# Optimization experiments

Measured on AMD Instinct MI355X. Metric: run time of the kernel, lower is better.

The kernel has to match this reference:

```python
import jax, jax.numpy as jnp
import numpy as np
import math

B, S, D, H, HD, W, G = 2, 4096, 768, 12, 64, 256, 64  # batch, seq, embed, heads, head_dim, one-sided window, n global tokens


def _chunk_keys(k, w):
    # k: [B,S,H,HD] -> overlapping 3w-wide key windows per w-sized query chunk: [B,nc,3w,H,HD]
    Bz, S_, Hh, HDd = k.shape
    nc = S_ // w
    kp = jnp.pad(k, ((0, 0), (w, w), (0, 0), (0, 0)))
    kb = kp.reshape(Bz, nc + 2, w, Hh, HDd)
    return jnp.concatenate([kb[:, 0:nc], kb[:, 1:nc + 1], kb[:, 2:nc + 2]], axis=2)


def _band_qk(q, k, w):
    # banded scores: out[b,i,h,j] = q_i . k_{i+j-w}, j in [0, 2w]
    Bz, S_, Hh, HDd = q.shape
    nc = S_ // w
    qc = q.reshape(Bz, nc, w, Hh, HDd)
    kc = _chunk_keys(k, w)
    sc = jnp.einsum('bcphd,bckhd->bchpk', qc, kc)  # [B,nc,H,w,3w]
    rows = jnp.arange(w)[:, None]
    cols = rows + jnp.arange(2 * w + 1)[None, :]   # within-window key index = p + j
    band = sc[:, :, :, rows, cols]                 # [B,nc,H,w,2w+1]
    return band.transpose(0, 1, 3, 2, 4).reshape(Bz, S_, Hh, 2 * w + 1)


def _band_pv(p, v, w):
    # out[b,i,h,:] = sum_j p[b,i,h,j] * v[b, i+j-w, h, :]
    Bz, S_, Hh, K = p.shape
    HDd = v.shape[-1]
    nc = S_ // w
    pc = p.reshape(Bz, nc, w, Hh, K).transpose(0, 1, 3, 2, 4)  # [B,nc,H,w,2w+1]
    rows = jnp.arange(w)[:, None]
    cols = rows + jnp.arange(2 * w + 1)[None, :]
    full = jnp.zeros((Bz, nc, Hh, w, 3 * w), p.dtype).at[:, :, :, rows, cols].set(pc)
    vc = _chunk_keys(v, w)
    out = jnp.einsum('bchpk,bckhd->bcphd', full, vc)  # [B,nc,w,H,HD]
    return out.reshape(Bz, S_, Hh, HDd)


def setup_inputs() -> dict:
    key = jax.random.key(0)
    ks = jax.random.split(key, 4)
    std = 0.02
    # attention mask: +1 = global (first G tokens), 0 = local windowed, no padding
    attention_mask = jnp.concatenate(
        [jnp.ones((B, G), jnp.int32), jnp.zeros((B, S - G), jnp.int32)], axis=1)
    return {
        'hidden_states': jax.random.normal(ks[0], (B, S, D), jnp.float32),
        'attention_mask': attention_mask,
        'Wq': jax.random.normal(ks[1], (D, D), jnp.float32) * std,
        'bq': jnp.zeros((D,), jnp.float32),
        'Wk': jax.random.normal(ks[2], (D, D), jnp.float32) * std,
        'bk': jnp.zeros((D,), jnp.float32),
        'Wv': jax.random.normal(ks[3], (D, D), jnp.float32) * std,
        'bv': jnp.zeros((D,), jnp.float32),
    }


def reference(hidden_states, attention_mask, Wq, bq, Wk, bk, Wv, bv):
    Bz, S_, D_ = hidden_states.shape
    HDd = D_ // H
    q = ((hidden_states @ Wq.T + bq) / math.sqrt(HDd)).reshape(Bz, S_, H, HDd)
    k = (hidden_states @ Wk.T + bk).reshape(Bz, S_, H, HDd)
    v = (hidden_states @ Wv.T + bv).reshape(Bz, S_, H, HDd)

    band = _band_qk(q, k, W)  # [B,S,H,2W+1]

    i = jnp.arange(S_)
    key_abs = i[:, None] + jnp.arange(2 * W + 1)[None, :] - W  # [S,2W+1]
    valid = (key_abs >= 0) & (key_abs < S_)
    kac = jnp.clip(key_abs, 0, S_ - 1)
    is_glob = attention_mask != 0                       # [B,S]
    glob_at_key = is_glob[:, kac] & valid[None]          # [B,S,2W+1]
    # remove global keys from windowed attention: d_mask = -10000 * head_dim (ones @ float_mask)
    band = band + jnp.where(glob_at_key, jnp.float32(-10000.0 * HDd), jnp.float32(0.0))[:, :, None, :]
    # mask_invalid_locations: out-of-range diagonals -> -inf
    band = jnp.where(valid[None, :, None, :], band, -jnp.inf)

    # global-token attention (first G tokens are the global ones)
    gs = jnp.einsum('bihd,bghd->bihg', q, k[:, :G])      # [B,S,H,G]

    scores = jnp.concatenate([gs, band], axis=-1)        # [B,S,H,G+2W+1]
    probs = jax.nn.softmax(scores.astype(jnp.float32), axis=-1)

    attn = jnp.einsum('bihg,bghd->bihd', probs[..., :G], v[:, :G]) + _band_pv(probs[..., G:], v, W)
    # [B,S,H,HD] -> (seq_len, bsz, embed_dim) as in the torch module
    return jnp.transpose(attn, (1, 0, 2, 3)).reshape(S_, Bz, D_)
```

## Files before the change

kernel.cpp:

```cpp
#include <hip/hip_runtime.h>
#include <hip/hip_bf16.h>
#include <stdint.h>

typedef __attribute__((ext_vector_type(4))) float          f32x4;
typedef __attribute__((ext_vector_type(4))) float          f4;
typedef __attribute__((ext_vector_type(2))) unsigned int   u32x2;
typedef __bf16 bf16_t;
typedef __attribute__((ext_vector_type(8))) bf16_t         bf16x8;
typedef __attribute__((ext_vector_type(8))) unsigned short u16x8;
typedef __attribute__((ext_vector_type(4))) unsigned short u16x4;

#define NB 2
#define NS 4096
#define ND 768
#define NH 12
#define NW 256

__device__ __forceinline__ unsigned short f2bf(float f) {
  union { float f; unsigned u; } v; v.f = f;
  unsigned r = v.u + 0x7fffu + ((v.u >> 16) & 1u);
  return (unsigned short)(r >> 16);
}

__device__ __forceinline__ void gload16(const void* g, void* l) {
  __builtin_amdgcn_global_load_lds((const __attribute__((address_space(1))) void*)g,
                                   (__attribute__((address_space(3))) void*)l, 16, 0, 0);
}

__global__ void cast_kernel(const float* __restrict__ in, unsigned short* __restrict__ out, int n4) {
  int i = blockIdx.x * blockDim.x + threadIdx.x;
  int stride = gridDim.x * blockDim.x;
  for (; i < n4; i += stride) {
    f4 v = reinterpret_cast<const f4*>(in)[i];
    unsigned u0 = (unsigned)f2bf(v.x) | ((unsigned)f2bf(v.y) << 16);
    unsigned u1 = (unsigned)f2bf(v.z) | ((unsigned)f2bf(v.w) << 16);
    u32x2 o = {u0, u1};
    reinterpret_cast<u32x2*>(out)[i] = o;
  }
}

__global__ void cast3_kernel(const float* __restrict__ w0, const float* __restrict__ w1,
                             const float* __restrict__ w2, unsigned short* __restrict__ o0,
                             unsigned short* __restrict__ o1, unsigned short* __restrict__ o2) {
  const int n4 = 768 * 768 / 4;
  int i = blockIdx.x * blockDim.x + threadIdx.x;
  int stride = gridDim.x * blockDim.x;
  for (; i < 3 * n4; i += stride) {
    int m = i / n4, j = i - m * n4;
    const float* in = (m == 0) ? w0 : ((m == 1) ? w1 : w2);
    unsigned short* out = (m == 0) ? o0 : ((m == 1) ? o1 : o2);
    f4 v = reinterpret_cast<const f4*>(in)[j];
    unsigned u0 = (unsigned)f2bf(v.x) | ((unsigned)f2bf(v.y) << 16);
    unsigned u1 = (unsigned)f2bf(v.z) | ((unsigned)f2bf(v.w) << 16);
    u32x2 o = {u0, u1};
    reinterpret_cast<u32x2*>(out)[j] = o;
  }
}

__global__ __launch_bounds__(256) void qkv_gemm(
    const unsigned short* __restrict__ Ab,
    const unsigned short* __restrict__ Wqb,
    const unsigned short* __restrict__ Wkb,
    const unsigned short* __restrict__ Wvb,
    const float* __restrict__ bqp, const float* __restrict__ bkp, const float* __restrict__ bvp,
    unsigned short* __restrict__ Qw, unsigned short* __restrict__ Kw, unsigned short* __restrict__ Vw) {
  __shared__ unsigned short As[128 * 32];
  __shared__ unsigned short Bs[128 * 32];

  int phys = blockIdx.x;
  int logical = (phys & 7) * 144 + (phys >> 3);
  int bn = logical % 18, bm = logical / 18;
  int mat = bn / 6, bnn = bn % 6;
  const unsigned short* Wm = (mat == 0) ? Wqb : ((mat == 1) ? Wkb : Wvb);
  const float* bias = (mat == 0) ? bqp : ((mat == 1) ? bkp : bvp);
  unsigned short* dst = (mat == 0) ? Qw : ((mat == 1) ? Kw : Vw);

  int t = threadIdx.x;
  int w = t >> 6, l = t & 63;
  int lg = l >> 4, ln = l & 15;
  int wm = w & 1, wn = w >> 1;

  f32x4 acc[4][4];
#pragma unroll
  for (int i = 0; i < 4; i++)
#pragma unroll
    for (int j = 0; j < 4; j++) acc[i][j] = f32x4{0.f, 0.f, 0.f, 0.f};

  for (int kt = 0; kt < 24; ++kt) {
    __syncthreads();
#pragma unroll
    for (int is = 0; is < 2; ++is) {
      int chunk = is * 256 + t;
      int row = chunk >> 2;
      int c8 = (chunk & 3) * 8;
      gload16(Ab + ((size_t)(bm * 128 + row)) * 768 + kt * 32 + c8, As + chunk * 8);
      gload16(Wm + ((size_t)(bnn * 128 + row)) * 768 + kt * 32 + c8, Bs + chunk * 8);
    }
    __syncthreads();
    bf16x8 af[4], bfr[4];
#pragma unroll
    for (int i = 0; i < 4; i++) {
      af[i]  = *reinterpret_cast<const bf16x8*>(As + (wm * 64 + i * 16 + ln) * 32 + lg * 8);
      bfr[i] = *reinterpret_cast<const bf16x8*>(Bs + (wn * 64 + i * 16 + ln) * 32 + lg * 8);
    }
#pragma unroll
    for (int i = 0; i < 4; i++)
#pragma unroll
      for (int j = 0; j < 4; j++)
        acc[i][j] = __builtin_amdgcn_mfma_f32_16x16x32_bf16(af[i], bfr[j], acc[i][j], 0, 0, 0);
  }

#pragma unroll
  for (int j = 0; j < 4; j++) {
    int col = bnn * 128 + wn * 64 + j * 16 + ln;
    float bv_ = bias[col];
    int hh = col >> 6, dd = col & 63;
#pragma unroll
    for (int i = 0; i < 4; i++) {
#pragma unroll
      for (int r = 0; r < 4; r++) {
        int tok = bm * 128 + wm * 64 + i * 16 + lg * 4 + r;
        int bb = tok >> 12, ss = tok & 4095;
        float v = acc[i][j][r] + bv_;
        if (mat == 0) v *= 0.125f;
        dst[(((size_t)bb * 12 + hh) * 4096 + ss) * 64 + dd] = f2bf(v);
      }
    }
  }
}

__global__ __launch_bounds__(512) void attn_kernel(
    const unsigned short* __restrict__ Qw,
    const unsigned short* __restrict__ Kw,
    const unsigned short* __restrict__ Vw,
    const int* __restrict__ amask,
    float* __restrict__ out) {
  __shared__ unsigned short Ks[2][64 * 64];
  __shared__ unsigned short Vt[2][64 * 64];
  __shared__ unsigned short Ps[8][16 * 72];
  __shared__ unsigned Msk[128];

  int phys = blockIdx.x;
  int logical = (phys & 7) * 96 + (phys >> 3);
  int qc = logical & 31;
  int bh = logical >> 5;
  int b = bh / 12;
  int hh = bh % 12;
  int qbase = qc * 128;

  int t = threadIdx.x, w = t >> 6, l = t & 63;
  int lg = l >> 4, ln = l & 15;

  const unsigned short* Qbh = Qw + (size_t)bh * (NS * 64);
  const unsigned short* Kbh = Kw + (size_t)bh * (NS * 64);
  const unsigned short* Vbh = Vw + (size_t)bh * (NS * 64);
  const int* mrow = amask + b * NS;

#pragma unroll
  for (int r8 = 0; r8 < 8; ++r8) {
    int wp = r8 * 8 + w;
    unsigned long long bal = __ballot(mrow[wp * 64 + l] != 0);
    if (l == 0) {
      Msk[wp * 2] = (unsigned)bal;
      Msk[wp * 2 + 1] = (unsigned)(bal >> 32);
    }
  }

  bf16x8 qf[2];
  {
    const unsigned short* qp = Qbh + (size_t)(qbase + w * 16 + ln) * 64 + lg * 8;
    qf[0] = *reinterpret_cast<const bf16x8*>(qp);
    qf[1] = *reinterpret_cast<const bf16x8*>(qp + 32);
  }

  float m_r[4] = {-1e30f, -1e30f, -1e30f, -1e30f};
  float l_r[4] = {0.f, 0.f, 0.f, 0.f};
  f32x4 oacc[4];
#pragma unroll
  for (int i = 0; i < 4; i++) oacc[i] = f32x4{0.f, 0.f, 0.f, 0.f};

  int q0 = qbase + w * 16 + lg * 4;

  int tt_lo = (qbase >= 256) ? 0 : ((256 - qbase) >> 6);
  int tt_hi_raw = (NS + 192 - qbase) >> 6;
  int tt_hi = tt_hi_raw < 9 ? tt_hi_raw : 9;
  int ntl = tt_hi - tt_lo + 2;

  int krow = t >> 3, gran = t & 7;
  int p2 = t & 31, d0v = (t >> 5) * 4;

  {
    gload16(Kbh + (size_t)krow * 64 + (gran ^ (krow & 7)) * 8, &Ks[0][0] + t * 8);
    const unsigned short* vp0 = Vbh + (size_t)(2 * p2) * 64 + d0v;
    u16x4 va = *reinterpret_cast<const u16x4*>(vp0);
    u16x4 vb = *reinterpret_cast<const u16x4*>(vp0 + 64);
#pragma unroll
    for (int j = 0; j < 4; ++j) {
      int d = d0v + j;
      unsigned val = (unsigned)va[j] | ((unsigned)vb[j] << 16);
      *reinterpret_cast<unsigned*>(&Vt[0][0] + d * 64 + ((2 * p2) ^ ((d & 7) << 3))) = val;
    }
  }
  __syncthreads();

  for (int idx = 0; idx < ntl; ++idx) {
    int cur = idx & 1;
    int key0 = (idx == 0) ? 0 : (qbase - 256 + (tt_lo + idx - 1) * 64);
    bool has_next = (idx + 1) < ntl;

    u16x4 va, vb;
    if (has_next) {
      int nk0 = qbase - 256 + (tt_lo + idx) * 64;
      gload16(Kbh + (size_t)(nk0 + krow) * 64 + (gran ^ (krow & 7)) * 8,
              &Ks[cur ^ 1][0] + t * 8);
      const unsigned short* vp0 = Vbh + (size_t)(nk0 + 2 * p2) * 64 + d0v;
      va = *reinterpret_cast<const u16x4*>(vp0);
      vb = *reinterpret_cast<const u16x4*>(vp0 + 64);
    }

    const unsigned short* ksb = &Ks[cur][0];
    f32x4 sa[4];
#pragma unroll
    for (int nt = 0; nt < 4; nt++) sa[nt] = f32x4{0.f, 0.f, 0.f, 0.f};
#pragma unroll
    for (int nt = 0; nt < 4; nt++) {
      int key = nt * 16 + ln;
#pragma unroll
      for (int ks = 0; ks < 2; ++ks) {
        int dby = (ks * 64 + lg * 16) ^ ((key & 7) << 4);
        bf16x8 kf = *reinterpret_cast<const bf16x8*>(ksb + key * 64 + (dby >> 1));
        sa[nt] = __builtin_amdgcn_mfma_f32_16x16x32_bf16(qf[ks], kf, sa[nt], 0, 0, 0);
      }
    }

    if (idx > 0) {
#pragma unroll
      for (int nt = 0; nt < 4; nt++) {
        int ka = key0 + nt * 16 + ln;
        bool sup = (Msk[ka >> 5] >> (ka & 31)) & 1;
#pragma unroll
        for (int r = 0; r < 4; r++) {
          bool bad = sup || ((unsigned)(ka - (q0 + r) + NW) > 2u * NW);
          if (bad) sa[nt][r] = -1e30f;
        }
      }
    }

    float scl[4];
#pragma unroll
    for (int r = 0; r < 4; r++) {
      float v = fmaxf(fmaxf(sa[0][r], sa[1][r]), fmaxf(sa[2][r], sa[3][r]));
      v = fmaxf(v, __shfl_xor(v, 1, 64));
      v = fmaxf(v, __shfl_xor(v, 2, 64));
      v = fmaxf(v, __shfl_xor(v, 4, 64));
      v = fmaxf(v, __shfl_xor(v, 8, 64));
      float mn = fmaxf(m_r[r], v);
      scl[r] = __expf(m_r[r] - mn);
      m_r[r] = mn;
    }
#pragma unroll
    for (int r = 0; r < 4; r++) {
      float s = 0.f;
#pragma unroll
      for (int nt = 0; nt < 4; nt++) {
        float p = __expf(sa[nt][r] - m_r[r]);
        sa[nt][r] = p;
        s += p;
      }
      s += __shfl_xor(s, 1, 64);
      s += __shfl_xor(s, 2, 64);
      s += __shfl_xor(s, 4, 64);
      s += __shfl_xor(s, 8, 64);
      l_r[r] = l_r[r] * scl[r] + s;
    }
#pragma unroll
    for (int nt = 0; nt < 4; nt++)
#pragma unroll
      for (int r = 0; r < 4; r++) oacc[nt][r] *= scl[r];

    unsigned short* pw = &Ps[w][0];
#pragma unroll
    for (int nt = 0; nt < 4; nt++)
#pragma unroll
      for (int r = 0; r < 4; r++) {
        __hip_bfloat16 hb = __float2bfloat16(sa[nt][r]);
        pw[(lg * 4 + r) * 72 + nt * 16 + ln] = *reinterpret_cast<unsigned short*>(&hb);
      }

    const unsigned short* vtb = &Vt[cur][0];
#pragma unroll
    for (int ks = 0; ks < 2; ++ks) {
      bf16x8 pf = *reinterpret_cast<const bf16x8*>(pw + ln * 72 + ks * 32 + lg * 8);
#pragma unroll
      for (int nt = 0; nt < 4; ++nt) {
        int d = nt * 16 + ln;
        int eoff = (ks * 32 + lg * 8) ^ ((d & 7) << 3);
        bf16x8 vf = *reinterpret_cast<const bf16x8*>(vtb + d * 64 + eoff);
        oacc[nt] = __builtin_amdgcn_mfma_f32_16x16x32_bf16(pf, vf, oacc[nt], 0, 0, 0);
      }
    }

    if (has_next) {
      unsigned short* vtn = &Vt[cur ^ 1][0];
#pragma unroll
      for (int j = 0; j < 4; ++j) {
        int d = d0v + j;
        unsigned val = (unsigned)va[j] | ((unsigned)vb[j] << 16);
        *reinterpret_cast<unsigned*>(vtn + d * 64 + ((2 * p2) ^ ((d & 7) << 3))) = val;
      }
    }
    __syncthreads();
  }

#pragma unroll
  for (int nt = 0; nt < 4; nt++) {
    int d = nt * 16 + ln;
#pragma unroll
    for (int r = 0; r < 4; r++) {
      int qa = q0 + r;
      out[((size_t)qa * NB + b) * ND + hh * 64 + d] = oacc[nt][r] / l_r[r];
    }
  }
}

extern "C" void kernel_launch(void* const* d_in, const int* in_sizes, int n_in,
                              void* d_out, int out_size, void* d_ws, size_t ws_size,
                              hipStream_t stream) {
  (void)in_sizes; (void)n_in; (void)out_size; (void)ws_size;
  const float* hidden = (const float*)d_in[0];
  const int*   amask  = (const int*)d_in[1];
  const float* Wq = (const float*)d_in[2];
  const float* bq = (const float*)d_in[3];
  const float* Wk = (const float*)d_in[4];
  const float* bk = (const float*)d_in[5];
  const float* Wv = (const float*)d_in[6];
  const float* bv = (const float*)d_in[7];
  float* out = (float*)d_out;

  char* p = (char*)d_ws;
  unsigned short* hb  = (unsigned short*)p; p += (size_t)8192 * 768 * 2;
  unsigned short* wqb = (unsigned short*)p; p += (size_t)768 * 768 * 2;
  unsigned short* wkb = (unsigned short*)p; p += (size_t)768 * 768 * 2;
  unsigned short* wvb = (unsigned short*)p; p += (size_t)768 * 768 * 2;
  unsigned short* Qws = (unsigned short*)p; p += (size_t)24 * 4096 * 64 * 2;
  unsigned short* Kws = (unsigned short*)p; p += (size_t)24 * 4096 * 64 * 2;
  unsigned short* Vws = (unsigned short*)p; p += (size_t)24 * 4096 * 64 * 2;

  cast_kernel<<<1024, 256, 0, stream>>>(hidden, hb, 8192 * 768 / 4);
  cast3_kernel<<<432, 256, 0, stream>>>(Wq, Wk, Wv, wqb, wkb, wvb);
  qkv_gemm<<<64 * 18, 256, 0, stream>>>(hb, wqb, wkb, wvb, bq, bk, bv, Qws, Kws, Vws);
  attn_kernel<<<24 * 32, 512, 0, stream>>>(Qws, Kws, Vws, amask, out);
}
```

Before: 209.7 us.

## Transpose attention MFMAs to keep P in registers and skip clean masks

Swaps MFMA operands so each lane owns one query row. Softmax stats become per-lane scalars, and P can be packed to bf16 in registers and fed to the PV MFMA without the LDS round trip. It folds log2(e) into the Q scale to use exp2f, adds a lazy rescale that only updates the running max when it grows by more than 8, and skips per-element masking for key tiles fully inside the window with no global keys. Output is written as float4 rows. The lazy-rescale threshold and the bf16 P values are numerics risks, and V reads become two 8-byte LDS loads instead of one 16-byte load.

```diff
diff --git a/kernel.cpp b/kernel.cpp
--- a/kernel.cpp
+++ b/kernel.cpp
@@ -22,6 +22,10 @@
   return (unsigned short)(r >> 16);
 }
 
+__device__ __forceinline__ unsigned pack2bf(float a, float b) {
+  return (unsigned)f2bf(a) | ((unsigned)f2bf(b) << 16);
+}
+
 __device__ __forceinline__ void gload16(const void* g, void* l) {
   __builtin_amdgcn_global_load_lds((const __attribute__((address_space(1))) void*)g,
                                    (__attribute__((address_space(3))) void*)l, 16, 0, 0);
@@ -32,9 +36,7 @@
   int stride = gridDim.x * blockDim.x;
   for (; i < n4; i += stride) {
     f4 v = reinterpret_cast<const f4*>(in)[i];
-    unsigned u0 = (unsigned)f2bf(v.x) | ((unsigned)f2bf(v.y) << 16);
-    unsigned u1 = (unsigned)f2bf(v.z) | ((unsigned)f2bf(v.w) << 16);
-    u32x2 o = {u0, u1};
+    u32x2 o = {pack2bf(v.x, v.y), pack2bf(v.z, v.w)};
     reinterpret_cast<u32x2*>(out)[i] = o;
   }
 }
@@ -50,9 +52,7 @@
     const float* in = (m == 0) ? w0 : ((m == 1) ? w1 : w2);
     unsigned short* out = (m == 0) ? o0 : ((m == 1) ? o1 : o2);
     f4 v = reinterpret_cast<const f4*>(in)[j];
-    unsigned u0 = (unsigned)f2bf(v.x) | ((unsigned)f2bf(v.y) << 16);
-    unsigned u1 = (unsigned)f2bf(v.z) | ((unsigned)f2bf(v.w) << 16);
-    u32x2 o = {u0, u1};
+    u32x2 o = {pack2bf(v.x, v.y), pack2bf(v.z, v.w)};
     reinterpret_cast<u32x2*>(out)[j] = o;
   }
 }
@@ -122,7 +122,7 @@
         int tok = bm * 128 + wm * 64 + i * 16 + lg * 4 + r;
         int bb = tok >> 12, ss = tok & 4095;
         float v = acc[i][j][r] + bv_;
-        if (mat == 0) v *= 0.125f;
+        if (mat == 0) v *= 0.1803368801111244f;
         dst[(((size_t)bb * 12 + hh) * 4096 + ss) * 64 + dd] = f2bf(v);
       }
     }
@@ -137,7 +137,6 @@
     float* __restrict__ out) {
   __shared__ unsigned short Ks[2][64 * 64];
   __shared__ unsigned short Vt[2][64 * 64];
-  __shared__ unsigned short Ps[8][16 * 72];
   __shared__ unsigned Msk[128];
 
   int phys = blockIdx.x;
@@ -166,20 +165,20 @@
     }
   }
 
+  int q = qbase + w * 16 + ln;
+  int qwmin = qbase + w * 16;
+
   bf16x8 qf[2];
   {
-    const unsigned short* qp = Qbh + (size_t)(qbase + w * 16 + ln) * 64 + lg * 8;
+    const unsigned short* qp = Qbh + (size_t)q * 64 + lg * 8;
     qf[0] = *reinterpret_cast<const bf16x8*>(qp);
     qf[1] = *reinterpret_cast<const bf16x8*>(qp + 32);
   }
 
-  float m_r[4] = {-1e30f, -1e30f, -1e30f, -1e30f};
-  float l_r[4] = {0.f, 0.f, 0.f, 0.f};
+  float m_s = -1e30f, l_s = 0.f;
   f32x4 oacc[4];
 #pragma unroll
   for (int i = 0; i < 4; i++) oacc[i] = f32x4{0.f, 0.f, 0.f, 0.f};
-
-  int q0 = qbase + w * 16 + lg * 4;
 
   int tt_lo = (qbase >= 256) ? 0 : ((256 - qbase) >> 6);
   int tt_hi_raw = (NS + 192 - qbase) >> 6;
@@ -229,74 +228,81 @@
       for (int ks = 0; ks < 2; ++ks) {
         int dby = (ks * 64 + lg * 16) ^ ((key & 7) << 4);
         bf16x8 kf = *reinterpret_cast<const bf16x8*>(ksb + key * 64 + (dby >> 1));
-        sa[nt] = __builtin_amdgcn_mfma_f32_16x16x32_bf16(qf[ks], kf, sa[nt], 0, 0, 0);
+        sa[nt] = __builtin_amdgcn_mfma_f32_16x16x32_bf16(kf, qf[ks], sa[nt], 0, 0, 0);
       }
     }
 
     if (idx > 0) {
-#pragma unroll
-      for (int nt = 0; nt < 4; nt++) {
-        int ka = key0 + nt * 16 + ln;
-        bool sup = (Msk[ka >> 5] >> (ka & 31)) & 1;
-#pragma unroll
-        for (int r = 0; r < 4; r++) {
-          bool bad = sup || ((unsigned)(ka - (q0 + r) + NW) > 2u * NW);
-          if (bad) sa[nt][r] = -1e30f;
+      unsigned mw0 = Msk[key0 >> 5], mw1 = Msk[(key0 >> 5) + 1];
+      bool clean = ((mw0 | mw1) == 0) && (key0 >= qwmin - 241) && (key0 <= qwmin + 193);
+      if (!clean) {
+#pragma unroll
+        for (int nt = 0; nt < 4; nt++) {
+          unsigned mword = (nt & 2) ? mw1 : mw0;
+#pragma unroll
+          for (int r = 0; r < 4; r++) {
+            int key = key0 + 16 * nt + 4 * lg + r;
+            bool sup = (mword >> ((16 * (nt & 1) + 4 * lg + r) & 31)) & 1;
+            bool bad = sup || ((unsigned)(key - q + NW) > 2u * NW);
+            if (bad) sa[nt][r] = -1e30f;
+          }
         }
       }
     }
 
-    float scl[4];
-#pragma unroll
-    for (int r = 0; r < 4; r++) {
-      float v = fmaxf(fmaxf(sa[0][r], sa[1][r]), fmaxf(sa[2][r], sa[3][r]));
-      v = fmaxf(v, __shfl_xor(v, 1, 64));
-      v = fmaxf(v, __shfl_xor(v, 2, 64));
-      v = fmaxf(v, __shfl_xor(v, 4, 64));
-      v = fmaxf(v, __shfl_xor(v, 8, 64));
-      float mn = fmaxf(m_r[r], v);
-      scl[r] = __expf(m_r[r] - mn);
-      m_r[r] = mn;
-    }
-#pragma unroll
-    for (int r = 0; r < 4; r++) {
-      float s = 0.f;
-#pragma unroll
-      for (int nt = 0; nt < 4; nt++) {
-        float p = __expf(sa[nt][r] - m_r[r]);
+    float tmax = sa[0][0];
+#pragma unroll
+    for (int nt = 0; nt < 4; nt++)
+#pragma unroll
+      for (int r = 0; r < 4; r++) tmax = fmaxf(tmax, sa[nt][r]);
+    tmax = fmaxf(tmax, __shfl_xor(tmax, 16, 64));
+    tmax = fmaxf(tmax, __shfl_xor(tmax, 32, 64));
+    if (!__all(tmax - m_s <= 8.f)) {
+      float mn = fmaxf(m_s, tmax);
+      float scl = exp2f(m_s - mn);
+      m_s = mn;
+      l_s *= scl;
+#pragma unroll
+      for (int i = 0; i < 4; i++) oacc[i] *= scl;
+    }
+    float ssum = 0.f;
+#pragma unroll
+    for (int nt = 0; nt < 4; nt++)
+#pragma unroll
+      for (int r = 0; r < 4; r++) {
+        float p = exp2f(sa[nt][r] - m_s);
         sa[nt][r] = p;
-        s += p;
-      }
-      s += __shfl_xor(s, 1, 64);
-      s += __shfl_xor(s, 2, 64);
-      s += __shfl_xor(s, 4, 64);
-      s += __shfl_xor(s, 8, 64);
-      l_r[r] = l_r[r] * scl[r] + s;
-    }
-#pragma unroll
-    for (int nt = 0; nt < 4; nt++)
-#pragma unroll
-      for (int r = 0; r < 4; r++) oacc[nt][r] *= scl[r];
-
-    unsigned short* pw = &Ps[w][0];
-#pragma unroll
-    for (int nt = 0; nt < 4; nt++)
-#pragma unroll
-      for (int r = 0; r < 4; r++) {
-        __hip_bfloat16 hb = __float2bfloat16(sa[nt][r]);
-        pw[(lg * 4 + r) * 72 + nt * 16 + ln] = *reinterpret_cast<unsigned short*>(&hb);
-      }
+        ssum += p;
+      }
+    ssum += __shfl_xor(ssum, 16, 64);
+    ssum += __shfl_xor(ssum, 32, 64);
+    l_s += ssum;
+
+    unsigned pk[4][2];
+#pragma unroll
+    for (int nt = 0; nt < 4; nt++) {
+      pk[nt][0] = pack2bf(sa[nt][0], sa[nt][1]);
+      pk[nt][1] = pack2bf(sa[nt][2], sa[nt][3]);
+    }
 
     const unsigned short* vtb = &Vt[cur][0];
 #pragma unroll
     for (int ks = 0; ks < 2; ++ks) {
-      bf16x8 pf = *reinterpret_cast<const bf16x8*>(pw + ln * 72 + ks * 32 + lg * 8);
+      union { unsigned u[4]; bf16x8 v; } pf;
+      pf.u[0] = pk[2 * ks][0];
+      pf.u[1] = pk[2 * ks][1];
+      pf.u[2] = pk[2 * ks + 1][0];
+      pf.u[3] = pk[2 * ks + 1][1];
 #pragma unroll
       for (int nt = 0; nt < 4; ++nt) {
         int d = nt * 16 + ln;
-        int eoff = (ks * 32 + lg * 8) ^ ((d & 7) << 3);
-        bf16x8 vf = *reinterpret_cast<const bf16x8*>(vtb + d * 64 + eoff);
-        oacc[nt] = __builtin_amdgcn_mfma_f32_16x16x32_bf16(pf, vf, oacc[nt], 0, 0, 0);
+        int sw = (d & 7) << 3;
+        int e0 = (32 * ks + 4 * lg) ^ sw;
+        int e1 = (32 * ks + 16 + 4 * lg) ^ sw;
+        union { u16x4 h[2]; bf16x8 v; } vf;
+        vf.h[0] = *reinterpret_cast<const u16x4*>(vtb + d * 64 + e0);
+        vf.h[1] = *reinterpret_cast<const u16x4*>(vtb + d * 64 + e1);
+        oacc[nt] = __builtin_amdgcn_mfma_f32_16x16x32_bf16(vf.v, pf.v, oacc[nt], 0, 0, 0);
       }
     }
 
@@ -312,14 +318,14 @@
     __syncthreads();
   }
 
+  float inv = 1.0f / l_s;
+  float* orow = out + ((size_t)q * NB + b) * ND + hh * 64;
 #pragma unroll
   for (int nt = 0; nt < 4; nt++) {
-    int d = nt * 16 + ln;
-#pragma unroll
-    for (int r = 0; r < 4; r++) {
-      int qa = q0 + r;
-      out[((size_t)qa * NB + b) * ND + hh * 64 + d] = oacc[nt][r] / l_r[r];
-    }
+    f4 o;
+#pragma unroll
+    for (int r = 0; r < 4; r++) o[r] = oacc[nt][r] * inv;
+    *reinterpret_cast<f4*>(orow + nt * 16 + 4 * lg) = o;
   }
 }
 
```

After: 201.6 us. 1.04x faster.
